# Kernel tuning notes

Hardware: AMD Instinct MI355X
Metric: run time of the kernel (lower is better)

## Reference

```python
import jax, jax.numpy as jnp
import numpy as np

N, E, D, K = 50000, 600000, 128, 8
EPS = 1e-09


def setup_inputs() -> dict:
    key = jax.random.key(0)
    ks = jax.random.split(key, 10)
    feature = jax.random.normal(ks[0], (N, D), dtype=jnp.float32)
    snorm_n = jax.random.uniform(ks[1], (N, 1), dtype=jnp.float32)
    src = jax.random.randint(ks[2], (E,), 0, N, dtype=jnp.int32)
    dst = jax.random.randint(ks[3], (E,), 0, N, dtype=jnp.int32)
    W_low = jax.random.normal(ks[4], (D, D), dtype=jnp.float32) / np.sqrt(D)
    W_high = jax.random.normal(ks[5], (D, D), dtype=jnp.float32) / np.sqrt(D)
    W_mid = jax.random.normal(ks[6], (D, D), dtype=jnp.float32) / np.sqrt(D)
    gamma_low = jax.random.uniform(ks[7], (K,), dtype=jnp.float32)
    gamma_high = jax.random.uniform(ks[8], (K,), dtype=jnp.float32)
    gamma_mid = jax.random.uniform(ks[9], (K,), dtype=jnp.float32)
    bias = jnp.zeros((D,), dtype=jnp.float32)
    return {"feature": feature, "snorm_n": snorm_n, "src": src, "dst": dst,
            "W_low": W_low, "W_high": W_high, "W_mid": W_mid,
            "gamma_low": gamma_low, "gamma_high": gamma_high,
            "gamma_mid": gamma_mid, "bias": bias}


def _mp(feat, src, dst, norm):
    # symmetric-normalized SpMM: h[v] = norm[v] * sum_{u->v} norm[u]*feat[u]
    msg = (feat * norm[:, None])[src]                        # [E, D] gather
    agg = jax.ops.segment_sum(msg, dst, num_segments=N)       # [N, D] scatter-add
    return agg * norm[:, None]


def reference(feature, snorm_n, src, dst, W_low, W_high, W_mid,
              gamma_low, gamma_high, gamma_mid, bias):
    deg = jax.ops.segment_sum(jnp.ones((E,), feature.dtype), dst, num_segments=N)
    norm = jnp.clip(deg, 1.0) ** -0.5                          # in-degree^-0.5
    alpha = jnp.linspace(EPS, 1.0 - EPS, K).astype(feature.dtype)
    midalpha = jnp.linspace(EPS, 1.0, K).astype(feature.dtype)

    h = _mp(feature, src, dst, norm)

    gl = jax.nn.relu(gamma_low)
    o0 = (jnp.dot(alpha, gl) * h + jnp.dot(1.0 - alpha, gl) * feature) @ W_low.T
    gh = jax.nn.relu(gamma_high)
    o1 = (jnp.dot(-alpha, gh) * h + jnp.dot(1.0 - alpha, gh) * feature) @ W_high.T
    gm = jax.nn.relu(gamma_mid)
    h1 = _mp(h, src, dst, norm)
    o2 = (jnp.sum(gm) * h1 - jnp.dot(midalpha, gm) * feature) @ W_mid.T

    # sequential mutual gating, exactly as the torch in-place updates
    o0 = o0 * jax.nn.sigmoid(o1 + o2)
    o1 = o1 * jax.nn.sigmoid(o0 + o2)
    o2 = o2 * jax.nn.sigmoid(o0 + o1)

    out = o0 + o1 + o2 + bias
    out = out * snorm_n          # graph_norm
    out = jax.nn.relu(out)       # activation
    return out
```

## Files before the change

kernel.cpp:

```cpp
#include <hip/hip_runtime.h>
#include <hip/hip_bf16.h>
#include <math.h>

#define N_NODES 50000
#define N_EDGES 600000
#define DIM 128
#define KGAM 8
#define EPSV 1e-9f
#define RBLK 3128

typedef __attribute__((ext_vector_type(8))) short short8;
typedef __attribute__((ext_vector_type(4))) float float4v;

__device__ __forceinline__ short f2bf(float f) {
    return (short)__builtin_bit_cast(unsigned short, __float2bfloat16(f));
}
__device__ __forceinline__ unsigned int pack2(float a, float b) {
    return (unsigned int)(unsigned short)f2bf(a) | ((unsigned int)(unsigned short)f2bf(b) << 16);
}
__device__ __forceinline__ float sigm(float x) { return 1.f / (1.f + __expf(-x)); }

__global__ void k_deg(const int* __restrict__ dst, int* __restrict__ deg) {
    int e = blockIdx.x * blockDim.x + threadIdx.x;
    if (e < N_EDGES) atomicAdd(&deg[dst[e]], 1);
}

__global__ void k_scan1(const int* __restrict__ deg, int* __restrict__ rowstart,
                        int* __restrict__ bsums, float* __restrict__ norm) {
    __shared__ int s[256];
    int tid = threadIdx.x;
    int i0 = blockIdx.x * 1024 + tid * 4;
    int v[4]; int sum = 0;
#pragma unroll
    for (int c = 0; c < 4; ++c) {
        int i = i0 + c;
        int d = (i < N_NODES) ? deg[i] : 0;
        v[c] = d; sum += d;
    }
    s[tid] = sum; __syncthreads();
#pragma unroll
    for (int off = 1; off < 256; off <<= 1) {
        int t = (tid >= off) ? s[tid - off] : 0;
        __syncthreads();
        s[tid] += t;
        __syncthreads();
    }
    if (tid == 255) bsums[blockIdx.x] = s[255];
    int run = s[tid] - sum;
#pragma unroll
    for (int c = 0; c < 4; ++c) {
        int i = i0 + c;
        if (i < N_NODES) {
            rowstart[i] = run;
            norm[i] = rsqrtf((float)(v[c] < 1 ? 1 : v[c]));
        }
        run += v[c];
    }
}

__global__ void k_scan2(int* __restrict__ bsums, int nb) {
    __shared__ int s[64];
    int tid = threadIdx.x;
    int v = (tid < nb) ? bsums[tid] : 0;
    s[tid] = v; __syncthreads();
#pragma unroll
    for (int off = 1; off < 64; off <<= 1) {
        int t = (tid >= off) ? s[tid - off] : 0;
        __syncthreads();
        s[tid] += t;
        __syncthreads();
    }
    if (tid < nb) bsums[tid] = s[tid] - v;
}

__global__ void k_scan3(const int* __restrict__ bsums, int* __restrict__ rowstart) {
    int i = blockIdx.x * blockDim.x + threadIdx.x;
    if (i < N_NODES) rowstart[i] += bsums[i >> 10];
    if (i == 0) rowstart[N_NODES] = N_EDGES;
}

__global__ void k_fill(const int* __restrict__ src, const int* __restrict__ dst,
                       const int* __restrict__ rowstart, int* __restrict__ cnt,
                       int* __restrict__ esrc) {
    int e = blockIdx.x * blockDim.x + threadIdx.x;
    if (e < N_EDGES) {
        int d = dst[e];
        int slot = rowstart[d] + atomicAdd(&cnt[d], 1);
        esrc[slot] = src[e];
    }
}

__global__ void k_wconv(const float* __restrict__ W0, const float* __restrict__ W1,
                        const float* __restrict__ W2, const float* __restrict__ gl,
                        const float* __restrict__ gh, const float* __restrict__ gm,
                        unsigned int* __restrict__ Wb) {
    int g = blockIdx.y;
    float a0 = 0, b0 = 0, a1 = 0, b1 = 0, sg = 0, m2 = 0;
#pragma unroll
    for (int k = 0; k < KGAM; ++k) {
        float al = EPSV + (float)k * (1.f - 2.f * EPSV) / (KGAM - 1);
        float md = EPSV + (float)k * (1.f - EPSV) / (KGAM - 1);
        float l = fmaxf(gl[k], 0.f), h = fmaxf(gh[k], 0.f), m = fmaxf(gm[k], 0.f);
        a0 += al * l;  b0 += (1.f - al) * l;
        a1 += -al * h; b1 += (1.f - al) * h;
        sg += m;       m2 += md * m;
    }
    float cc[6] = {a0, b0, a1, b1, sg, -m2};
    float c = cc[g];
    const float* Ws = (g < 2) ? W0 : (g < 4) ? W1 : W2;
    int i = (blockIdx.x * 256 + threadIdx.x) * 4;
    if (i < DIM * DIM) {
        float4 v = *(const float4*)(Ws + i);
        uint2 o; o.x = pack2(c * v.x, c * v.y); o.y = pack2(c * v.z, c * v.w);
        *(uint2*)(Wb + (g * DIM * DIM + i) / 2) = o;
    }
}

__device__ __forceinline__ size_t tiled_off(int row, int k) {
    return (size_t)(row >> 4) * 2048 + ((k >> 5) << 9) + (((k >> 3) & 3) << 7)
         + ((row & 15) << 3) + (k & 7);
}

__global__ void k_prescale(const float4* __restrict__ f, const float* __restrict__ norm,
                           unsigned int* __restrict__ fb, uint2* __restrict__ fp) {
    int i = blockIdx.x * 256 + threadIdx.x;
    if (i >= N_NODES * DIM / 4) return;
    int row = i >> 5;
    int k0 = (i & 31) * 4;
    float nv = norm[row];
    float4 v = f[i];
    uint2 a; a.x = pack2(v.x, v.y); a.y = pack2(v.z, v.w);
    uint2 b; b.x = pack2(v.x * nv, v.y * nv); b.y = pack2(v.z * nv, v.w * nv);
    *(uint2*)(fb + tiled_off(row, k0) / 2) = a;
    fp[i] = b;
}

__device__ __forceinline__ void acc8(float* a, uint4 r) {
    a[0] += __builtin_bit_cast(float, r.x << 16);
    a[1] += __builtin_bit_cast(float, r.x & 0xffff0000u);
    a[2] += __builtin_bit_cast(float, r.y << 16);
    a[3] += __builtin_bit_cast(float, r.y & 0xffff0000u);
    a[4] += __builtin_bit_cast(float, r.z << 16);
    a[5] += __builtin_bit_cast(float, r.z & 0xffff0000u);
    a[6] += __builtin_bit_cast(float, r.w << 16);
    a[7] += __builtin_bit_cast(float, r.w & 0xffff0000u);
}

__global__ void k_spmm(const uint4* __restrict__ in, const float* __restrict__ norm,
                       const int* __restrict__ rowstart, const int* __restrict__ esrc,
                       uint4* __restrict__ hout, uint4* __restrict__ preout, int wpre) {
    int v = blockIdx.x * 16 + (threadIdx.x >> 4);
    int l = threadIdx.x & 15;
    if (v >= N_NODES) return;
    int beg = rowstart[v], end = rowstart[v + 1];
    float a[8] = {0.f, 0.f, 0.f, 0.f, 0.f, 0.f, 0.f, 0.f};
    int t = beg;
    for (; t + 7 < end; t += 8) {
        int u0 = esrc[t],     u1 = esrc[t + 1], u2 = esrc[t + 2], u3 = esrc[t + 3];
        int u4 = esrc[t + 4], u5 = esrc[t + 5], u6 = esrc[t + 6], u7 = esrc[t + 7];
        uint4 r0 = in[(size_t)u0 * 16 + l];
        uint4 r1 = in[(size_t)u1 * 16 + l];
        uint4 r2 = in[(size_t)u2 * 16 + l];
        uint4 r3 = in[(size_t)u3 * 16 + l];
        uint4 r4 = in[(size_t)u4 * 16 + l];
        uint4 r5 = in[(size_t)u5 * 16 + l];
        uint4 r6 = in[(size_t)u6 * 16 + l];
        uint4 r7 = in[(size_t)u7 * 16 + l];
        acc8(a, r0); acc8(a, r1); acc8(a, r2); acc8(a, r3);
        acc8(a, r4); acc8(a, r5); acc8(a, r6); acc8(a, r7);
    }
    if (t + 3 < end) {
        int u0 = esrc[t], u1 = esrc[t + 1], u2 = esrc[t + 2], u3 = esrc[t + 3];
        uint4 r0 = in[(size_t)u0 * 16 + l];
        uint4 r1 = in[(size_t)u1 * 16 + l];
        uint4 r2 = in[(size_t)u2 * 16 + l];
        uint4 r3 = in[(size_t)u3 * 16 + l];
        acc8(a, r0); acc8(a, r1); acc8(a, r2); acc8(a, r3);
        t += 4;
    }
    if (t + 1 < end) {
        int u0 = esrc[t], u1 = esrc[t + 1];
        uint4 r0 = in[(size_t)u0 * 16 + l];
        uint4 r1 = in[(size_t)u1 * 16 + l];
        acc8(a, r0); acc8(a, r1);
        t += 2;
    }
    if (t < end) {
        uint4 r = in[(size_t)esrc[t] * 16 + l];
        acc8(a, r);
    }
    float nv = norm[v];
    uint4 o;
    o.x = pack2(a[0] * nv, a[1] * nv); o.y = pack2(a[2] * nv, a[3] * nv);
    o.z = pack2(a[4] * nv, a[5] * nv); o.w = pack2(a[6] * nv, a[7] * nv);
    size_t tix = (size_t)(v >> 4) * 256 + (size_t)(l >> 2) * 64
               + (size_t)(l & 3) * 16 + (v & 15);
    hout[tix] = o;
    if (wpre) {
        float n2 = nv * nv;
        uint4 p;
        p.x = pack2(a[0] * n2, a[1] * n2); p.y = pack2(a[2] * n2, a[3] * n2);
        p.z = pack2(a[4] * n2, a[5] * n2); p.w = pack2(a[6] * n2, a[7] * n2);
        preout[(size_t)v * 16 + l] = p;
    }
}

#define RT 64

typedef const __attribute__((address_space(1))) unsigned int* gp1_t;
typedef __attribute__((address_space(3))) unsigned int* lp3_t;

__global__ __launch_bounds__(512, 4) void k_gemm_fused(
    const short* __restrict__ hB, const short* __restrict__ fB,
    const short* __restrict__ h1B, const short* __restrict__ Wb,
    const float* __restrict__ bias, const float* __restrict__ snorm,
    float* __restrict__ out) {
    __shared__ short Ts[48 * 512];

    const int r0 = blockIdx.x * RT;
    const int tid = threadIdx.x;
    const int lane = tid & 63;
    const int wv = tid >> 6;
    const int m = lane & 15;
    const int quad = lane >> 4;

#pragma unroll
    for (int i = 0; i < 6; ++i) {
        int s = wv * 6 + i;
        int g = s >> 4, rt = (s >> 2) & 3, ks = s & 3;
        const short* base = (g == 0) ? hB : (g == 1) ? fB : h1B;
        const short* gp = base + (size_t)((r0 >> 4) + rt) * 2048 + ks * 512 + lane * 8;
        __builtin_amdgcn_global_load_lds((gp1_t)(const void*)gp,
                                         (lp3_t)(void*)&Ts[s * 512], 16, 0, 0);
    }
    __syncthreads();

    float4v acc[3][4];
    const float4v zero = {0.f, 0.f, 0.f, 0.f};
#pragma unroll
    for (int g = 0; g < 3; ++g)
#pragma unroll
        for (int rt = 0; rt < 4; ++rt) acc[g][rt] = zero;

    const short* wp = Wb + (size_t)(wv * 16 + m) * DIM + quad * 8;
#pragma unroll
    for (int ks = 0; ks < 4; ++ks) {
        const int ko = ks * 32;
        short8 b0 = *(const short8*)(wp + ko);
        short8 b1 = *(const short8*)(wp + ko + DIM * DIM);
        short8 b2 = *(const short8*)(wp + ko + 2 * DIM * DIM);
        short8 b3 = *(const short8*)(wp + ko + 3 * DIM * DIM);
        short8 b4 = *(const short8*)(wp + ko + 4 * DIM * DIM);
        short8 b5 = *(const short8*)(wp + ko + 5 * DIM * DIM);
#pragma unroll
        for (int rt = 0; rt < 4; ++rt) {
            const short* ap = &Ts[(rt * 4 + ks) * 512 + lane * 8];
            short8 x_h = *(const short8*)(ap);
            short8 x_f = *(const short8*)(ap + 16 * 512);
            short8 x_1 = *(const short8*)(ap + 32 * 512);
            acc[0][rt] = __builtin_amdgcn_mfma_f32_16x16x32_bf16(x_h, b0, acc[0][rt], 0, 0, 0);
            acc[0][rt] = __builtin_amdgcn_mfma_f32_16x16x32_bf16(x_f, b1, acc[0][rt], 0, 0, 0);
            acc[1][rt] = __builtin_amdgcn_mfma_f32_16x16x32_bf16(x_h, b2, acc[1][rt], 0, 0, 0);
            acc[1][rt] = __builtin_amdgcn_mfma_f32_16x16x32_bf16(x_f, b3, acc[1][rt], 0, 0, 0);
            acc[2][rt] = __builtin_amdgcn_mfma_f32_16x16x32_bf16(x_1, b4, acc[2][rt], 0, 0, 0);
            acc[2][rt] = __builtin_amdgcn_mfma_f32_16x16x32_bf16(x_f, b5, acc[2][rt], 0, 0, 0);
        }
    }

    const int col = wv * 16 + m;
    const float bc = bias[col];
#pragma unroll
    for (int rt = 0; rt < 4; ++rt) {
#pragma unroll
        for (int r = 0; r < 4; ++r) {
            int row = r0 + rt * 16 + quad * 4 + r;
            if (row < N_NODES) {
                float sn = snorm[row];
                float o0 = acc[0][rt][r], o1 = acc[1][rt][r], o2 = acc[2][rt][r];
                float g0 = o0 * sigm(o1 + o2);
                float g1 = o1 * sigm(g0 + o2);
                float g2 = o2 * sigm(g0 + g1);
                float vv = (g0 + g1 + g2 + bc) * sn;
                out[(size_t)row * DIM + col] = fmaxf(vv, 0.f);
            }
        }
    }
}

extern "C" void kernel_launch(void* const* d_in, const int* in_sizes, int n_in,
                              void* d_out, int out_size, void* d_ws, size_t ws_size,
                              hipStream_t stream) {
    const float* feature = (const float*)d_in[0];
    const float* snorm   = (const float*)d_in[1];
    const int*   src     = (const int*)d_in[2];
    const int*   dst     = (const int*)d_in[3];
    const float* W_low   = (const float*)d_in[4];
    const float* W_high  = (const float*)d_in[5];
    const float* W_mid   = (const float*)d_in[6];
    const float* gl      = (const float*)d_in[7];
    const float* gh      = (const float*)d_in[8];
    const float* gm      = (const float*)d_in[9];
    const float* bias    = (const float*)d_in[10];
    float* out = (float*)d_out;

    char* w = (char*)d_ws;
    auto alloc = [&](size_t bytes) {
        char* p = w;
        w += (bytes + 255) & ~(size_t)255;
        return p;
    };
    const size_t tiledBytes = (size_t)RBLK * 2048 * 2;
    float* norm   = (float*)alloc((size_t)N_NODES * 4);
    int* deg      = (int*)alloc((size_t)2 * N_NODES * 4);
    int* cnt      = deg + N_NODES;
    int* rowstart = (int*)alloc((size_t)(N_NODES + 1) * 4);
    int* bsums    = (int*)alloc(64 * 4);
    int* esrc     = (int*)alloc((size_t)N_EDGES * 4);
    short* Wb     = (short*)alloc((size_t)6 * DIM * DIM * 2);
    short* fb     = (short*)alloc(tiledBytes);
    short* fp     = (short*)alloc((size_t)N_NODES * DIM * 2);
    short* h      = (short*)alloc(tiledBytes);
    short* hp     = (short*)alloc((size_t)N_NODES * DIM * 2);
    short* h1     = (short*)alloc(tiledBytes);

    hipMemsetAsync(deg, 0, (size_t)2 * N_NODES * 4, stream);
    k_deg<<<(N_EDGES + 255) / 256, 256, 0, stream>>>(dst, deg);
    int nchunks = (N_NODES + 1023) / 1024;
    k_scan1<<<nchunks, 256, 0, stream>>>(deg, rowstart, bsums, norm);
    k_scan2<<<1, 64, 0, stream>>>(bsums, nchunks);
    k_scan3<<<(N_NODES + 255) / 256, 256, 0, stream>>>(bsums, rowstart);
    k_fill<<<(N_EDGES + 255) / 256, 256, 0, stream>>>(src, dst, rowstart, cnt, esrc);
    k_wconv<<<dim3(16, 6), 256, 0, stream>>>(W_low, W_high, W_mid, gl, gh, gm,
                                             (unsigned int*)Wb);
    k_prescale<<<(N_NODES * DIM / 4 + 255) / 256, 256, 0, stream>>>(
        (const float4*)feature, norm, (unsigned int*)fb, (uint2*)fp);

    int spmm_blocks = (N_NODES + 15) / 16;
    k_spmm<<<spmm_blocks, 256, 0, stream>>>((const uint4*)fp, norm, rowstart, esrc,
                                            (uint4*)h, (uint4*)hp, 1);
    k_spmm<<<spmm_blocks, 256, 0, stream>>>((const uint4*)hp, norm, rowstart, esrc,
                                            (uint4*)h1, (uint4*)hp, 0);

    k_gemm_fused<<<(N_NODES + RT - 1) / RT, 512, 0, stream>>>(
        h, fb, h1, Wb, bias, snorm, out);
}
```

Baseline: 255.8 us.

## Make fused GEMM persistent with double-buffered LDS prefetch of row tiles

The fused gating GEMM is now a persistent kernel with a fixed grid of 512 blocks. Each block loops over 32-row tiles and prefetches the next tile's h, feature and h1 bf16 slices into a second LDS buffer while it computes the current one. The intent is to hide global-load latency and to avoid launching and setting up many short-lived blocks. In exchange, tiles shrink from 64 to 32 rows, the kernel relies on a single barrier per iteration, and occupancy per CU is lowered.

```diff
diff --git a/kernel.cpp b/kernel.cpp
--- a/kernel.cpp
+++ b/kernel.cpp
@@ -8,6 +8,8 @@
 #define KGAM 8
 #define EPSV 1e-9f
 #define RBLK 3128
+#define NTILES 1564
+#define GGRID 512
 
 typedef __attribute__((ext_vector_type(8))) short short8;
 typedef __attribute__((ext_vector_type(4))) float float4v;
@@ -205,85 +207,104 @@
     }
 }
 
-#define RT 64
-
 typedef const __attribute__((address_space(1))) unsigned int* gp1_t;
 typedef __attribute__((address_space(3))) unsigned int* lp3_t;
 
-__global__ __launch_bounds__(512, 4) void k_gemm_fused(
+__global__ __launch_bounds__(512, 2) void k_gemm_fused(
     const short* __restrict__ hB, const short* __restrict__ fB,
     const short* __restrict__ h1B, const short* __restrict__ Wb,
     const float* __restrict__ bias, const float* __restrict__ snorm,
     float* __restrict__ out) {
-    __shared__ short Ts[48 * 512];
-
-    const int r0 = blockIdx.x * RT;
+    __shared__ short Ts[2][24 * 512];
+
     const int tid = threadIdx.x;
     const int lane = tid & 63;
     const int wv = tid >> 6;
     const int m = lane & 15;
     const int quad = lane >> 4;
 
-#pragma unroll
-    for (int i = 0; i < 6; ++i) {
-        int s = wv * 6 + i;
-        int g = s >> 4, rt = (s >> 2) & 3, ks = s & 3;
-        const short* base = (g == 0) ? hB : (g == 1) ? fB : h1B;
-        const short* gp = base + (size_t)((r0 >> 4) + rt) * 2048 + ks * 512 + lane * 8;
-        __builtin_amdgcn_global_load_lds((gp1_t)(const void*)gp,
-                                         (lp3_t)(void*)&Ts[s * 512], 16, 0, 0);
-    }
-    __syncthreads();
-
-    float4v acc[3][4];
-    const float4v zero = {0.f, 0.f, 0.f, 0.f};
-#pragma unroll
-    for (int g = 0; g < 3; ++g)
-#pragma unroll
-        for (int rt = 0; rt < 4; ++rt) acc[g][rt] = zero;
-
-    const short* wp = Wb + (size_t)(wv * 16 + m) * DIM + quad * 8;
-#pragma unroll
-    for (int ks = 0; ks < 4; ++ks) {
-        const int ko = ks * 32;
-        short8 b0 = *(const short8*)(wp + ko);
-        short8 b1 = *(const short8*)(wp + ko + DIM * DIM);
-        short8 b2 = *(const short8*)(wp + ko + 2 * DIM * DIM);
-        short8 b3 = *(const short8*)(wp + ko + 3 * DIM * DIM);
-        short8 b4 = *(const short8*)(wp + ko + 4 * DIM * DIM);
-        short8 b5 = *(const short8*)(wp + ko + 5 * DIM * DIM);
-#pragma unroll
-        for (int rt = 0; rt < 4; ++rt) {
-            const short* ap = &Ts[(rt * 4 + ks) * 512 + lane * 8];
-            short8 x_h = *(const short8*)(ap);
-            short8 x_f = *(const short8*)(ap + 16 * 512);
-            short8 x_1 = *(const short8*)(ap + 32 * 512);
-            acc[0][rt] = __builtin_amdgcn_mfma_f32_16x16x32_bf16(x_h, b0, acc[0][rt], 0, 0, 0);
-            acc[0][rt] = __builtin_amdgcn_mfma_f32_16x16x32_bf16(x_f, b1, acc[0][rt], 0, 0, 0);
-            acc[1][rt] = __builtin_amdgcn_mfma_f32_16x16x32_bf16(x_h, b2, acc[1][rt], 0, 0, 0);
-            acc[1][rt] = __builtin_amdgcn_mfma_f32_16x16x32_bf16(x_f, b3, acc[1][rt], 0, 0, 0);
-            acc[2][rt] = __builtin_amdgcn_mfma_f32_16x16x32_bf16(x_1, b4, acc[2][rt], 0, 0, 0);
-            acc[2][rt] = __builtin_amdgcn_mfma_f32_16x16x32_bf16(x_f, b5, acc[2][rt], 0, 0, 0);
-        }
-    }
-
     const int col = wv * 16 + m;
     const float bc = bias[col];
-#pragma unroll
-    for (int rt = 0; rt < 4; ++rt) {
-#pragma unroll
-        for (int r = 0; r < 4; ++r) {
-            int row = r0 + rt * 16 + quad * 4 + r;
-            if (row < N_NODES) {
-                float sn = snorm[row];
-                float o0 = acc[0][rt][r], o1 = acc[1][rt][r], o2 = acc[2][rt][r];
-                float g0 = o0 * sigm(o1 + o2);
-                float g1 = o1 * sigm(g0 + o2);
-                float g2 = o2 * sigm(g0 + g1);
-                float vv = (g0 + g1 + g2 + bc) * sn;
-                out[(size_t)row * DIM + col] = fmaxf(vv, 0.f);
+    const short* wp = Wb + (size_t)col * DIM + quad * 8;
+
+    int t0 = blockIdx.x;
+    {
+#pragma unroll
+        for (int i = 0; i < 3; ++i) {
+            int s = wv * 3 + i;
+            int g = s >> 3, rb = (s >> 2) & 1, ks = s & 3;
+            const short* base = (g == 0) ? hB : (g == 1) ? fB : h1B;
+            const short* gp = base + (size_t)(t0 * 2 + rb) * 2048 + ks * 512 + lane * 8;
+            __builtin_amdgcn_global_load_lds((gp1_t)(const void*)gp,
+                                             (lp3_t)(void*)&Ts[0][s * 512], 16, 0, 0);
+        }
+    }
+
+    int buf = 0;
+    for (int t = t0; t < NTILES; t += GGRID) {
+        __syncthreads();
+
+        int tn = t + GGRID;
+        if (tn < NTILES) {
+#pragma unroll
+            for (int i = 0; i < 3; ++i) {
+                int s = wv * 3 + i;
+                int g = s >> 3, rb = (s >> 2) & 1, ks = s & 3;
+                const short* base = (g == 0) ? hB : (g == 1) ? fB : h1B;
+                const short* gp = base + (size_t)(tn * 2 + rb) * 2048 + ks * 512 + lane * 8;
+                __builtin_amdgcn_global_load_lds((gp1_t)(const void*)gp,
+                                                 (lp3_t)(void*)&Ts[buf ^ 1][s * 512], 16, 0, 0);
             }
         }
+
+        float4v acc[3][2];
+        const float4v zero = {0.f, 0.f, 0.f, 0.f};
+#pragma unroll
+        for (int g = 0; g < 3; ++g) {
+            acc[g][0] = zero; acc[g][1] = zero;
+        }
+
+#pragma unroll
+        for (int ks = 0; ks < 4; ++ks) {
+            const short* wk = wp + ks * 32;
+            short8 b0 = *(const short8*)(wk);
+            short8 b1 = *(const short8*)(wk + DIM * DIM);
+            short8 b2 = *(const short8*)(wk + 2 * DIM * DIM);
+            short8 b3 = *(const short8*)(wk + 3 * DIM * DIM);
+            short8 b4 = *(const short8*)(wk + 4 * DIM * DIM);
+            short8 b5 = *(const short8*)(wk + 5 * DIM * DIM);
+#pragma unroll
+            for (int rb = 0; rb < 2; ++rb) {
+                const short* ap = &Ts[buf][(rb * 4 + ks) * 512 + lane * 8];
+                short8 x_h = *(const short8*)(ap);
+                short8 x_f = *(const short8*)(ap + 8 * 512);
+                short8 x_1 = *(const short8*)(ap + 16 * 512);
+                acc[0][rb] = __builtin_amdgcn_mfma_f32_16x16x32_bf16(x_h, b0, acc[0][rb], 0, 0, 0);
+                acc[0][rb] = __builtin_amdgcn_mfma_f32_16x16x32_bf16(x_f, b1, acc[0][rb], 0, 0, 0);
+                acc[1][rb] = __builtin_amdgcn_mfma_f32_16x16x32_bf16(x_h, b2, acc[1][rb], 0, 0, 0);
+                acc[1][rb] = __builtin_amdgcn_mfma_f32_16x16x32_bf16(x_f, b3, acc[1][rb], 0, 0, 0);
+                acc[2][rb] = __builtin_amdgcn_mfma_f32_16x16x32_bf16(x_1, b4, acc[2][rb], 0, 0, 0);
+                acc[2][rb] = __builtin_amdgcn_mfma_f32_16x16x32_bf16(x_f, b5, acc[2][rb], 0, 0, 0);
+            }
+        }
+
+#pragma unroll
+        for (int rb = 0; rb < 2; ++rb) {
+#pragma unroll
+            for (int r = 0; r < 4; ++r) {
+                int row = t * 32 + rb * 16 + quad * 4 + r;
+                if (row < N_NODES) {
+                    float sn = snorm[row];
+                    float o0 = acc[0][rb][r], o1 = acc[1][rb][r], o2 = acc[2][rb][r];
+                    float g0 = o0 * sigm(o1 + o2);
+                    float g1 = o1 * sigm(g0 + o2);
+                    float g2 = o2 * sigm(g0 + g1);
+                    float vv = (g0 + g1 + g2 + bc) * sn;
+                    out[(size_t)row * DIM + col] = fmaxf(vv, 0.f);
+                }
+            }
+        }
+        buf ^= 1;
     }
 }
 
@@ -341,6 +362,5 @@
     k_spmm<<<spmm_blocks, 256, 0, stream>>>((const uint4*)hp, norm, rowstart, esrc,
                                             (uint4*)h1, (uint4*)hp, 0);
 
-    k_gemm_fused<<<(N_NODES + RT - 1) / RT, 512, 0, stream>>>(
-        h, fb, h1, Wb, bias, snorm, out);
-}
+    k_gemm_fused<<<GGRID, 512, 0, stream>>>(h, fb, h1, Wb, bias, snorm, out);
+}
```

After: 252.9 us. Within noise of the previous version (-1.1%).
